# Optimization experiments

Measured on AMD Instinct MI355X. Metric: run time of the kernel, lower is better.

## Reference

```python
import jax, jax.numpy as jnp
import numpy as np

B, S, E, H, Dh = 2, 2048, 1024, 16, 64


def setup_inputs() -> dict:
    key = jax.random.key(0)
    ks = jax.random.split(key, 8)
    w = 0.02
    return {
        "x": jax.random.normal(ks[0], (B, S, E), jnp.float32),
        # torch Linear convention: weight (out, in) = (Dh, E), stacked over heads
        "Wq": jax.random.normal(ks[1], (H, Dh, E), jnp.float32) * w,
        "bq": jax.random.normal(ks[2], (H, Dh), jnp.float32) * w,
        "Wk": jax.random.normal(ks[3], (H, Dh, E), jnp.float32) * w,
        "bk": jax.random.normal(ks[4], (H, Dh), jnp.float32) * w,
        "Wv": jax.random.normal(ks[5], (H, Dh, E), jnp.float32) * w,
        "bv": jax.random.normal(ks[6], (H, Dh), jnp.float32) * w,
        "proj": jax.random.normal(ks[7], (H * Dh, E), jnp.float32) * w,
    }


def reference(x, Wq, bq, Wk, bk, Wv, bv, proj):
    b, s, e = x.shape
    h, dh, _ = Wq.shape
    scale = jnp.sqrt(jnp.asarray(dh, x.dtype))
    # per-head linear projections: y = x @ W.T + b  -> (b, h, s, dh)
    q = jnp.einsum('bse,hde->bhsd', x, Wq) + bq[None, :, None, :]
    k = jnp.einsum('bse,hde->bhsd', x, Wk) + bk[None, :, None, :]
    v = jnp.einsum('bse,hde->bhsd', x, Wv) + bv[None, :, None, :]
    causal = jnp.triu(jnp.ones((s, s), bool), 1)
    scores = jnp.einsum('bhsd,bhtd->bhst', q, k) / scale
    scores = jnp.where(causal[None, None], -jnp.inf, scores)
    # quirk: softmax output divided by sqrt(head_size) a second time
    att = jax.nn.softmax(scores, axis=-1) / scale
    z = jnp.einsum('bhst,bhtd->bhsd', att, v)
    # quirk: torch reshapes (B,H,S,Dh) row-major into (B,S,H*Dh) WITHOUT transpose
    z = z.reshape(b, s, h * dh)
    return z @ proj
```

## Files before the change

kernel.cpp:

```cpp
#include <hip/hip_runtime.h>
#include <hip/hip_bf16.h>

typedef unsigned short u16;
typedef unsigned int u32;
typedef __bf16 bf16x8 __attribute__((ext_vector_type(8)));
typedef float f32x4 __attribute__((ext_vector_type(4)));
typedef u16 u16x8 __attribute__((ext_vector_type(8)));
typedef u16 u16x4 __attribute__((ext_vector_type(4)));
typedef u32 u32x4 __attribute__((ext_vector_type(4)));

#define B_ 2
#define S_ 2048
#define E_ 1024
#define H_ 16
#define Dh_ 64

static __device__ __forceinline__ u16 f2bf(float f) {
  unsigned u = __builtin_bit_cast(unsigned, f);
  u += 0x7fff + ((u >> 16) & 1);
  return (u16)(u >> 16);
}

static __device__ __forceinline__ void gload16(const u16* g, u16* l) {
  __builtin_amdgcn_global_load_lds((const __attribute__((address_space(1))) unsigned int*)g,
                                   (__attribute__((address_space(3))) unsigned int*)l,
                                   16, 0, 0);
}

__global__ void cvt_all(const float* __restrict__ x, const float* __restrict__ wq,
                        const float* __restrict__ wk, const float* __restrict__ wv,
                        u16* __restrict__ xb, u16* __restrict__ wcat) {
  const int i = blockIdx.x * 256 + threadIdx.x;
  const float* src; u16x8* dst;
  if (i < 524288) {
    src = x + (size_t)i * 8;            dst = (u16x8*)xb + i;
  } else {
    const int j = i - 524288;
    dst = (u16x8*)wcat + j;
    if (j < 131072)      src = wq + (size_t)j * 8;
    else if (j < 262144) src = wk + (size_t)(j - 131072) * 8;
    else                 src = wv + (size_t)(j - 262144) * 8;
  }
  float4 a = ((const float4*)src)[0], b = ((const float4*)src)[1];
  u16x8 o;
  o[0] = f2bf(a.x); o[1] = f2bf(a.y); o[2] = f2bf(a.z); o[3] = f2bf(a.w);
  o[4] = f2bf(b.x); o[5] = f2bf(b.y); o[6] = f2bf(b.z); o[7] = f2bf(b.w);
  *dst = o;
}

__global__ void transpose_cvt(const float* __restrict__ in, u16* __restrict__ outT) {
  __shared__ float t[32][33];
  const int e = blockIdx.x * 32 + threadIdx.x;
  const int f = blockIdx.y * 32 + threadIdx.y;
  t[threadIdx.y][threadIdx.x] = in[f * 1024 + e];
  __syncthreads();
  const int eo = blockIdx.x * 32 + threadIdx.y;
  const int fo = blockIdx.y * 32 + threadIdx.x;
  outT[eo * 1024 + fo] = f2bf(t[threadIdx.x][threadIdx.y]);
}

__global__ __launch_bounds__(256) void qkv_gemm(const u16* __restrict__ Wcat,
                                                const u16* __restrict__ Xm,
                                                const float* __restrict__ bq,
                                                const float* __restrict__ bk,
                                                const float* __restrict__ bv,
                                                u16* __restrict__ Qb, u16* __restrict__ Kb,
                                                u16* __restrict__ Vtb, float qs) {
  __shared__ __align__(16) u16 As[2][4096];
  __shared__ __align__(16) u16 Bs[2][4096];
  const int tid = threadIdx.x;
  const int wv = tid >> 6, ln = tid & 63;
  const int lq = ln & 15, lg = ln >> 4;
  const int bid = blockIdx.x;
  const int xcd = bid & 7, within = bid >> 3;
  const int bx = (xcd & 1) * 12 + within % 12;
  const int by = (xcd >> 1) * 8 + within / 12;
  const int ra0 = bx * 128, rb0 = by * 128;
  const int wra = wv >> 1, wrb = wv & 1;

  f32x4 acc[4][4];
  const f32x4 z4 = {0.f, 0.f, 0.f, 0.f};
#pragma unroll
  for (int i = 0; i < 4; ++i)
#pragma unroll
    for (int j = 0; j < 4; ++j) acc[i][j] = z4;

  const int arow = tid >> 2;
  const int acol = (tid & 3) * 8;
  const u16* Ags = Wcat + (ra0 + arow) * 1024 + acol;
  const u16* Bgs = Xm + (rb0 + arow) * 1024 + acol;

#define GSTAGE(KT, BUF) do { const int k0_ = (KT) * 32;              \
    gload16(Ags + k0_,         &As[BUF][wv * 512]);                  \
    gload16(Ags + 65536 + k0_, &As[BUF][wv * 512 + 2048]);           \
    gload16(Bgs + k0_,         &Bs[BUF][wv * 512]);                  \
    gload16(Bgs + 65536 + k0_, &Bs[BUF][wv * 512 + 2048]); } while (0)

  GSTAGE(0, 0);
  for (int kt = 0; kt < 32; ++kt) {
    const int cb = kt & 1;
    if (kt < 31) {
      GSTAGE(kt + 1, cb ^ 1);
      asm volatile("s_waitcnt vmcnt(4)" ::: "memory");
    } else {
      asm volatile("s_waitcnt vmcnt(0)" ::: "memory");
    }
    __builtin_amdgcn_s_barrier();
    __builtin_amdgcn_sched_barrier(0);
    bf16x8 af[4], bfr[4];
#pragma unroll
    for (int i = 0; i < 4; ++i)
      af[i] = *(const bf16x8*)&As[cb][(wra * 64 + i * 16 + lq) * 32 + lg * 8];
#pragma unroll
    for (int j = 0; j < 4; ++j)
      bfr[j] = *(const bf16x8*)&Bs[cb][(wrb * 64 + j * 16 + lq) * 32 + lg * 8];
#pragma unroll
    for (int i = 0; i < 4; ++i)
#pragma unroll
      for (int j = 0; j < 4; ++j)
        acc[i][j] = __builtin_amdgcn_mfma_f32_16x16x32_bf16(af[i], bfr[j], acc[i][j], 0, 0, 0);
    __builtin_amdgcn_sched_barrier(0);
    __builtin_amdgcn_s_barrier();
  }
#undef GSTAGE

  const int region = bx >> 3;
  const float* bias = (region == 0) ? bq : (region == 1) ? bk : bv;
  const float osc = (region == 0) ? qs : 1.0f;
  const int Ar = ra0 + wra * 64, Br = rb0 + wrb * 64;
#pragma unroll
  for (int i = 0; i < 4; ++i) {
#pragma unroll
    for (int j = 0; j < 4; ++j) {
      const int n0 = Ar + i * 16 + lg * 4;
      const int nl = n0 & 1023;
      const int h = nl >> 6, d = nl & 63;
      const int m = Br + j * 16 + lq;
      const int bb = m >> 11, s = m & 2047;
      const float4 b4 = *(const float4*)&bias[nl];
      if (region < 2) {
        u16* out = (region == 0) ? Qb : Kb;
        u16x4 pk;
        pk[0] = f2bf((acc[i][j][0] + b4.x) * osc);
        pk[1] = f2bf((acc[i][j][1] + b4.y) * osc);
        pk[2] = f2bf((acc[i][j][2] + b4.z) * osc);
        pk[3] = f2bf((acc[i][j][3] + b4.w) * osc);
        *(u16x4*)&out[((bb * H_ + h) * S_ + s) * Dh_ + d] = pk;
      } else {
        const float bvv[4] = {b4.x, b4.y, b4.z, b4.w};
#pragma unroll
        for (int r = 0; r < 4; ++r)
          Vtb[((bb * H_ + h) * Dh_ + d + r) * S_ + s] = f2bf(acc[i][j][r] + bvv[r]);
      }
    }
  }
}

__global__ __launch_bounds__(256) void proj_gemm(const u16* __restrict__ Am,
                                                 const u16* __restrict__ Bm,
                                                 float* __restrict__ out) {
  __shared__ __align__(16) u16 As[2][4096];
  __shared__ __align__(16) u16 Bs[2][2048];
  const int tid = threadIdx.x;
  const int wv = tid >> 6, ln = tid & 63;
  const int lq = ln & 15, lg = ln >> 4;
  const int bid = blockIdx.x;
  const int xcd = bid & 7, within = bid >> 3;
  const int bx = within & 7;
  const int by = xcd * 8 + (within >> 3);
  const int ra0 = bx * 128, rb0 = by * 64;
  const int wra = wv >> 1, wrb = wv & 1;

  f32x4 acc[4][2];
  const f32x4 z4 = {0.f, 0.f, 0.f, 0.f};
#pragma unroll
  for (int i = 0; i < 4; ++i)
#pragma unroll
    for (int j = 0; j < 2; ++j) acc[i][j] = z4;

  const int arow = tid >> 2;
  const int acol = (tid & 3) * 8;
  const int brow = wv * 16 + (ln >> 2);
  const int bcol = (ln & 3) * 8;
  const u16* Ags = Am + (ra0 + arow) * 1024 + acol;
  const u16* Bgs = Bm + (rb0 + brow) * 1024 + bcol;

#define PSTAGE(KT, BUF) do { const int k0_ = (KT) * 32;              \
    gload16(Ags + k0_,         &As[BUF][wv * 512]);                  \
    gload16(Ags + 65536 + k0_, &As[BUF][wv * 512 + 2048]);           \
    gload16(Bgs + k0_,         &Bs[BUF][wv * 512]); } while (0)

  PSTAGE(0, 0);
  for (int kt = 0; kt < 32; ++kt) {
    const int cb = kt & 1;
    if (kt < 31) {
      PSTAGE(kt + 1, cb ^ 1);
      asm volatile("s_waitcnt vmcnt(3)" ::: "memory");
    } else {
      asm volatile("s_waitcnt vmcnt(0)" ::: "memory");
    }
    __builtin_amdgcn_s_barrier();
    __builtin_amdgcn_sched_barrier(0);
    bf16x8 af[4], bfr[2];
#pragma unroll
    for (int i = 0; i < 4; ++i)
      af[i] = *(const bf16x8*)&As[cb][(wra * 64 + i * 16 + lq) * 32 + lg * 8];
#pragma unroll
    for (int j = 0; j < 2; ++j)
      bfr[j] = *(const bf16x8*)&Bs[cb][(wrb * 32 + j * 16 + lq) * 32 + lg * 8];
#pragma unroll
    for (int i = 0; i < 4; ++i)
#pragma unroll
      for (int j = 0; j < 2; ++j)
        acc[i][j] = __builtin_amdgcn_mfma_f32_16x16x32_bf16(af[i], bfr[j], acc[i][j], 0, 0, 0);
    __builtin_amdgcn_sched_barrier(0);
    __builtin_amdgcn_s_barrier();
  }
#undef PSTAGE

  const int Ar = ra0 + wra * 64, Br = rb0 + wrb * 32;
#pragma unroll
  for (int i = 0; i < 4; ++i)
#pragma unroll
    for (int j = 0; j < 2; ++j) {
      const int e0 = Ar + i * 16 + lg * 4;
      const int m = Br + j * 16 + lq;
      *(f32x4*)&out[m * 1024 + e0] = acc[i][j];
    }
}

__global__ __launch_bounds__(512, 4) void attn_kernel(const u16* __restrict__ Q,
                                                      const u16* __restrict__ K,
                                                      const u16* __restrict__ Vt,
                                                      u16* __restrict__ Z) {
  __shared__ __align__(16) u16 Ktile[2][8192];
  __shared__ __align__(16) u16 Vtile[2][8192];
  const int tid = threadIdx.x;
  const int wv = tid >> 6, ln = tid & 63;
  const int lq = ln & 15, lg = ln >> 4;
  const bool lgodd = (lg & 1) != 0;
  const int id = blockIdx.x;
  const int within = id >> 3;
  const int xg = id & 7;
  int bh, qt;
  if (within < 32) { bh = xg * 4 + (within >> 4);     qt = 15 - (within & 15); }
  else { const int w = within - 32; bh = xg * 4 + 2 + (w >> 4); qt = w & 15; }
  const int qrow = (qt << 7) + wv * 16 + lq;
  const u16* Qp = Q + (size_t)bh * S_ * Dh_;
  const u16* Kp = K + (size_t)bh * S_ * Dh_;
  const u16* Vp = Vt + (size_t)bh * Dh_ * S_;

  int kgofs[2], vgrow[2], vgcol[2];
#pragma unroll
  for (int j = 0; j < 2; ++j) {
    const int p = j * 512 + tid;
    const int gk = p ^ ((p >> 3) & 7);
    kgofs[j] = (gk >> 3) * 64 + (gk & 7) * 8;
    vgrow[j] = p >> 4;
    vgcol[j] = ((p & 15) ^ ((p >> 4) & 15)) * 8;
  }
  const int sc0 = (lg ^ (lq & 7)) * 8;
  const int sc1 = ((4 + lg) ^ (lq & 7)) * 8;

  bf16x8 qf0 = *(const bf16x8*)&Qp[qrow * Dh_ + lg * 8];
  bf16x8 qf1 = *(const bf16x8*)&Qp[qrow * Dh_ + 32 + lg * 8];

  f32x4 o[4];
  const f32x4 z4 = {0.f, 0.f, 0.f, 0.f};
#pragma unroll
  for (int dt = 0; dt < 4; ++dt) o[dt] = z4;
  float l_lane = 0.f;

#define STAGE(KT, BUF) do { const int kb_ = (KT) * 128;                              \
    gload16(Kp + (size_t)kb_ * 64 + kgofs[0], &Ktile[BUF][wv * 512]);                \
    gload16(Kp + (size_t)kb_ * 64 + kgofs[1], &Ktile[BUF][4096 + wv * 512]);         \
    gload16(Vp + (size_t)vgrow[0] * 2048 + kb_ + vgcol[0], &Vtile[BUF][wv * 512]);   \
    gload16(Vp + (size_t)vgrow[1] * 2048 + kb_ + vgcol[1], &Vtile[BUF][4096 + wv * 512]); \
  } while (0)

  STAGE(0, 0);

  int cur = 0;
  for (int kt = 0; kt <= qt; ++kt) {
    if (kt < qt) {
      STAGE(kt + 1, cur ^ 1);
      asm volatile("s_waitcnt vmcnt(4)" ::: "memory");
    } else {
      asm volatile("s_waitcnt vmcnt(0)" ::: "memory");
    }
    __builtin_amdgcn_s_barrier();
    __builtin_amdgcn_sched_barrier(0);
    const int k0 = kt * 128;
    const bool diag = (kt == qt);
    const int nkk = diag ? ((wv >> 1) + 1) : 4;
#pragma unroll
    for (int kk = 0; kk < 4; ++kk) {
      if (kk < nkk) {
        const int rA = (kk * 32 + lq) * 64;
        const int rB = rA + 1024;
        bf16x8 kA0 = *(const bf16x8*)&Ktile[cur][rA + sc0];
        bf16x8 kA1 = *(const bf16x8*)&Ktile[cur][rA + sc1];
        bf16x8 kB0 = *(const bf16x8*)&Ktile[cur][rB + sc0];
        bf16x8 kB1 = *(const bf16x8*)&Ktile[cur][rB + sc1];
        f32x4 sa = z4, sb = z4;
        __builtin_amdgcn_s_setprio(1);
        sa = __builtin_amdgcn_mfma_f32_16x16x32_bf16(kA0, qf0, sa, 0, 0, 0);
        sa = __builtin_amdgcn_mfma_f32_16x16x32_bf16(kA1, qf1, sa, 0, 0, 0);
        sb = __builtin_amdgcn_mfma_f32_16x16x32_bf16(kB0, qf0, sb, 0, 0, 0);
        sb = __builtin_amdgcn_mfma_f32_16x16x32_bf16(kB1, qf1, sb, 0, 0, 0);
        __builtin_amdgcn_s_setprio(0);
        if (diag) {
          const int keyA = k0 + kk * 32 + lg * 4;
          const int keyB = keyA + 16;
#pragma unroll
          for (int r = 0; r < 4; ++r) {
            if (keyA + r > qrow) sa[r] = -3.0e38f;
            if (keyB + r > qrow) sb[r] = -3.0e38f;
          }
        }
        float e0 = __builtin_amdgcn_exp2f(sa[0]);
        float e1 = __builtin_amdgcn_exp2f(sa[1]);
        float e2 = __builtin_amdgcn_exp2f(sa[2]);
        float e3 = __builtin_amdgcn_exp2f(sa[3]);
        float f0 = __builtin_amdgcn_exp2f(sb[0]);
        float f1 = __builtin_amdgcn_exp2f(sb[1]);
        float f2 = __builtin_amdgcn_exp2f(sb[2]);
        float f3 = __builtin_amdgcn_exp2f(sb[3]);
        l_lane += ((e0 + e1) + (e2 + e3)) + ((f0 + f1) + (f2 + f3));
        u32 A0, A1, B0, B1;
        asm("v_cvt_pk_bf16_f32 %0, %1, %2" : "=v"(A0) : "v"(e0), "v"(e1));
        asm("v_cvt_pk_bf16_f32 %0, %1, %2" : "=v"(A1) : "v"(e2), "v"(e3));
        asm("v_cvt_pk_bf16_f32 %0, %1, %2" : "=v"(B0) : "v"(f0), "v"(f1));
        asm("v_cvt_pk_bf16_f32 %0, %1, %2" : "=v"(B1) : "v"(f2), "v"(f3));
        asm("v_permlane32_swap_b32 %0, %1" : "+v"(A0), "+v"(B0));
        asm("v_permlane32_swap_b32 %0, %1" : "+v"(A1), "+v"(B1));
        const u32 A0x = __shfl_xor((int)A0, 16), B0x = __shfl_xor((int)B0, 16);
        const u32 A1x = __shfl_xor((int)A1, 16), B1x = __shfl_xor((int)B1, 16);
        u32x4 w;
        w[0] = lgodd ? B0x : A0;
        w[1] = lgodd ? B1x : A1;
        w[2] = lgodd ? B0 : A0x;
        w[3] = lgodd ? B1 : A1x;
        const bf16x8 pf = __builtin_bit_cast(bf16x8, w);
        const int scvk = ((kk * 4 + lg) ^ lq) * 8;
        __builtin_amdgcn_s_setprio(1);
#pragma unroll
        for (int dt = 0; dt < 4; ++dt) {
          bf16x8 vf = *(const bf16x8*)&Vtile[cur][(dt * 16 + lq) * 128 + scvk];
          o[dt] = __builtin_amdgcn_mfma_f32_16x16x32_bf16(vf, pf, o[dt], 0, 0, 0);
        }
        __builtin_amdgcn_s_setprio(0);
      }
    }
    __builtin_amdgcn_sched_barrier(0);
    __builtin_amdgcn_s_barrier();
    cur ^= 1;
  }
#undef STAGE

  float l = l_lane;
  l += __shfl_xor(l, 16);
  l += __shfl_xor(l, 32);
  const float inv = 0.125f / l;
#pragma unroll
  for (int dt = 0; dt < 4; ++dt) {
    u16x4 pko;
#pragma unroll
    for (int r = 0; r < 4; ++r) pko[r] = f2bf(o[dt][r] * inv);
    *(u16x4*)&Z[((size_t)bh * S_ + qrow) * Dh_ + dt * 16 + lg * 4] = pko;
  }
}

extern "C" void kernel_launch(void* const* d_in, const int* in_sizes, int n_in,
                              void* d_out, int out_size, void* d_ws, size_t ws_size,
                              hipStream_t stream) {
  const float* x    = (const float*)d_in[0];
  const float* Wq   = (const float*)d_in[1];
  const float* bq   = (const float*)d_in[2];
  const float* Wk   = (const float*)d_in[3];
  const float* bk   = (const float*)d_in[4];
  const float* Wv   = (const float*)d_in[5];
  const float* bv   = (const float*)d_in[6];
  const float* proj = (const float*)d_in[7];
  float* out = (float*)d_out;

  char* p = (char*)d_ws;
  u16* xb   = (u16*)p; p += (size_t)4096 * 1024 * 2;
  u16* wcat = (u16*)p; p += (size_t)3072 * 1024 * 2;
  u16* pjt  = (u16*)p; p += (size_t)1024 * 1024 * 2;
  u16* Qb   = (u16*)p; p += (size_t)4096 * 1024 * 2;
  u16* Kb   = (u16*)p; p += (size_t)4096 * 1024 * 2;
  u16* Vtb  = (u16*)p; p += (size_t)4096 * 1024 * 2;
  u16* Zb   = (u16*)p; p += (size_t)4096 * 1024 * 2;

  cvt_all<<<dim3(3584), dim3(256), 0, stream>>>(x, Wq, Wk, Wv, xb, wcat);
  transpose_cvt<<<dim3(32, 32), dim3(32, 32), 0, stream>>>(proj, pjt);

  const float qs = 0.125f * 1.44269504f;
  qkv_gemm<<<dim3(768), dim3(256), 0, stream>>>(wcat, xb, bq, bk, bv, Qb, Kb, Vtb, qs);

  attn_kernel<<<dim3(512), dim3(512), 0, stream>>>(Qb, Kb, Vtb, Zb);

  proj_gemm<<<dim3(512), dim3(256), 0, stream>>>(pjt, Zb, out);
}
```

Before: 105.0 us.

## Retile QKV GEMM to 256x256 blocks with swizzled LDS and interleaved pipeline

The QKV projection GEMM now uses 256x256 output tiles with 512 threads and a K step of 64, instead of 128x128 tiles with 256 threads. LDS columns are XOR-swizzled to avoid bank conflicts. The loop is split into four phases that interleave LDS reads, prefetching of the next stage and MFMA bursts, with raised priority during the MFMAs. The goal is more arithmetic per byte loaded and better overlap of loads with MFMAs. In exchange the grid shrinks to 192 blocks, fewer than the 256 CUs, and the double-buffered LDS grows to 128KB per block.

```diff
diff --git a/kernel.cpp b/kernel.cpp
--- a/kernel.cpp
+++ b/kernel.cpp
@@ -59,83 +59,130 @@
   outT[eo * 1024 + fo] = f2bf(t[threadIdx.x][threadIdx.y]);
 }
 
-__global__ __launch_bounds__(256) void qkv_gemm(const u16* __restrict__ Wcat,
-                                                const u16* __restrict__ Xm,
-                                                const float* __restrict__ bq,
-                                                const float* __restrict__ bk,
-                                                const float* __restrict__ bv,
-                                                u16* __restrict__ Qb, u16* __restrict__ Kb,
-                                                u16* __restrict__ Vtb, float qs) {
-  __shared__ __align__(16) u16 As[2][4096];
-  __shared__ __align__(16) u16 Bs[2][4096];
+__global__ __launch_bounds__(512, 2) void qkv_gemm(const u16* __restrict__ Wcat,
+                                                   const u16* __restrict__ Xm,
+                                                   const float* __restrict__ bq,
+                                                   const float* __restrict__ bk,
+                                                   const float* __restrict__ bv,
+                                                   u16* __restrict__ Qb, u16* __restrict__ Kb,
+                                                   u16* __restrict__ Vtb, float qs) {
+  __shared__ __align__(16) u16 Alds[2][16384];
+  __shared__ __align__(16) u16 Blds[2][16384];
   const int tid = threadIdx.x;
   const int wv = tid >> 6, ln = tid & 63;
   const int lq = ln & 15, lg = ln >> 4;
+  const int wm = wv >> 2, wn = wv & 3;
   const int bid = blockIdx.x;
-  const int xcd = bid & 7, within = bid >> 3;
-  const int bx = (xcd & 1) * 12 + within % 12;
-  const int by = (xcd >> 1) * 8 + within / 12;
-  const int ra0 = bx * 128, rb0 = by * 128;
-  const int wra = wv >> 1, wrb = wv & 1;
-
-  f32x4 acc[4][4];
+  const int xcd = bid & 7, w = bid >> 3;
+  const int bx = w % 12;
+  const int by = xcd * 2 + w / 12;
+  const int ra0 = bx * 256, rb0 = by * 256;
+
+  const int r_t = tid >> 3, c_t = tid & 7;
+  const int gcol = (c_t ^ (r_t & 7)) * 8;
+  const u16* Asrc = Wcat + (ra0 + r_t) * 1024 + gcol;
+  const u16* Bsrc = Xm   + (rb0 + r_t) * 1024 + gcol;
+
+  const int sc0 = (lg ^ (lq & 7)) * 8;
+  const int sc1 = ((4 + lg) ^ (lq & 7)) * 8;
+  const int baseA = (wm * 128 + lq) * 64;
+  const int baseB = (wn * 64 + lq) * 64;
+
+  f32x4 acc[8][4];
   const f32x4 z4 = {0.f, 0.f, 0.f, 0.f};
 #pragma unroll
-  for (int i = 0; i < 4; ++i)
+  for (int i = 0; i < 8; ++i)
 #pragma unroll
     for (int j = 0; j < 4; ++j) acc[i][j] = z4;
 
-  const int arow = tid >> 2;
-  const int acol = (tid & 3) * 8;
-  const u16* Ags = Wcat + (ra0 + arow) * 1024 + acol;
-  const u16* Bgs = Xm + (rb0 + arow) * 1024 + acol;
-
-#define GSTAGE(KT, BUF) do { const int k0_ = (KT) * 32;              \
-    gload16(Ags + k0_,         &As[BUF][wv * 512]);                  \
-    gload16(Ags + 65536 + k0_, &As[BUF][wv * 512 + 2048]);           \
-    gload16(Bgs + k0_,         &Bs[BUF][wv * 512]);                  \
-    gload16(Bgs + 65536 + k0_, &Bs[BUF][wv * 512 + 2048]); } while (0)
-
-  GSTAGE(0, 0);
-  for (int kt = 0; kt < 32; ++kt) {
-    const int cb = kt & 1;
-    if (kt < 31) {
-      GSTAGE(kt + 1, cb ^ 1);
-      asm volatile("s_waitcnt vmcnt(4)" ::: "memory");
-    } else {
-      asm volatile("s_waitcnt vmcnt(0)" ::: "memory");
-    }
-    __builtin_amdgcn_s_barrier();
-    __builtin_amdgcn_sched_barrier(0);
-    bf16x8 af[4], bfr[4];
-#pragma unroll
-    for (int i = 0; i < 4; ++i)
-      af[i] = *(const bf16x8*)&As[cb][(wra * 64 + i * 16 + lq) * 32 + lg * 8];
-#pragma unroll
-    for (int j = 0; j < 4; ++j)
-      bfr[j] = *(const bf16x8*)&Bs[cb][(wrb * 64 + j * 16 + lq) * 32 + lg * 8];
-#pragma unroll
-    for (int i = 0; i < 4; ++i)
-#pragma unroll
-      for (int j = 0; j < 4; ++j)
-        acc[i][j] = __builtin_amdgcn_mfma_f32_16x16x32_bf16(af[i], bfr[j], acc[i][j], 0, 0, 0);
-    __builtin_amdgcn_sched_barrier(0);
-    __builtin_amdgcn_s_barrier();
-  }
-#undef GSTAGE
-
-  const int region = bx >> 3;
+#define SA(Q, KT, BUF) gload16(Asrc + (Q) * 65536 + (KT) * 64, &Alds[BUF][((Q) * 512 + tid) * 8])
+#define SB(Q, KT, BUF) gload16(Bsrc + (Q) * 65536 + (KT) * 64, &Blds[BUF][((Q) * 512 + tid) * 8])
+#define LOADA(MH, SC) do {                                                         \
+    _Pragma("unroll") for (int ii = 0; ii < 4; ++ii)                               \
+      af[ii] = *(const bf16x8*)&Alds[cb][baseA + (MH) * 4096 + ii * 1024 + (SC)];  \
+  } while (0)
+#define LOADB(DST, SC) do {                                                        \
+    _Pragma("unroll") for (int j = 0; j < 4; ++j)                                  \
+      DST[j] = *(const bf16x8*)&Blds[cb][baseB + j * 1024 + (SC)];                 \
+  } while (0)
+#define MF(MH, BQ) do {                                                            \
+    _Pragma("unroll") for (int ii = 0; ii < 4; ++ii)                               \
+      _Pragma("unroll") for (int j = 0; j < 4; ++j)                                \
+        acc[(MH) * 4 + ii][j] =                                                    \
+            __builtin_amdgcn_mfma_f32_16x16x32_bf16(af[ii], BQ[j],                 \
+                                                    acc[(MH) * 4 + ii][j], 0, 0, 0); \
+  } while (0)
+
+  SB(0, 0, 0); SB(1, 0, 0); SB(2, 0, 0); SB(3, 0, 0);
+  SA(0, 0, 0); SA(2, 0, 0); SA(1, 0, 0); SA(3, 0, 0);
+
+  for (int kt = 0; kt < 16; ++kt) {
+    const int cb = kt & 1, nb = cb ^ 1;
+    const bool st = (kt < 15);
+    asm volatile("s_waitcnt vmcnt(2)" ::: "memory");
+    __builtin_amdgcn_s_barrier();
+    __builtin_amdgcn_sched_barrier(0);
+    bf16x8 af[4], bq0[4], bq1[4];
+    LOADA(0, sc0);
+    LOADB(bq0, sc0);
+    if (st) { SB(0, kt + 1, nb); SB(1, kt + 1, nb); }
+    __builtin_amdgcn_s_barrier();
+    asm volatile("s_waitcnt lgkmcnt(0)" ::: "memory");
+    __builtin_amdgcn_sched_barrier(0);
+    __builtin_amdgcn_s_setprio(1);
+    MF(0, bq0);
+    __builtin_amdgcn_s_setprio(0);
+    __builtin_amdgcn_s_barrier();
+    LOADA(0, sc1);
+    LOADB(bq1, sc1);
+    if (st) { SB(2, kt + 1, nb); SB(3, kt + 1, nb); }
+    __builtin_amdgcn_s_barrier();
+    asm volatile("s_waitcnt lgkmcnt(0)" ::: "memory");
+    __builtin_amdgcn_sched_barrier(0);
+    __builtin_amdgcn_s_setprio(1);
+    MF(0, bq1);
+    __builtin_amdgcn_s_setprio(0);
+    __builtin_amdgcn_s_barrier();
+    if (st) { asm volatile("s_waitcnt vmcnt(4)" ::: "memory"); }
+    else    { asm volatile("s_waitcnt vmcnt(0)" ::: "memory"); }
+    __builtin_amdgcn_s_barrier();
+    __builtin_amdgcn_sched_barrier(0);
+    LOADA(1, sc0);
+    if (st) { SA(0, kt + 1, nb); SA(2, kt + 1, nb); }
+    __builtin_amdgcn_s_barrier();
+    asm volatile("s_waitcnt lgkmcnt(0)" ::: "memory");
+    __builtin_amdgcn_sched_barrier(0);
+    __builtin_amdgcn_s_setprio(1);
+    MF(1, bq0);
+    __builtin_amdgcn_s_setprio(0);
+    __builtin_amdgcn_s_barrier();
+    LOADA(1, sc1);
+    if (st) { SA(1, kt + 1, nb); SA(3, kt + 1, nb); }
+    __builtin_amdgcn_s_barrier();
+    asm volatile("s_waitcnt lgkmcnt(0)" ::: "memory");
+    __builtin_amdgcn_sched_barrier(0);
+    __builtin_amdgcn_s_setprio(1);
+    MF(1, bq1);
+    __builtin_amdgcn_s_setprio(0);
+    __builtin_amdgcn_s_barrier();
+  }
+#undef SA
+#undef SB
+#undef LOADA
+#undef LOADB
+#undef MF
+
+  const int region = bx >> 2;
   const float* bias = (region == 0) ? bq : (region == 1) ? bk : bv;
   const float osc = (region == 0) ? qs : 1.0f;
-  const int Ar = ra0 + wra * 64, Br = rb0 + wrb * 64;
-#pragma unroll
-  for (int i = 0; i < 4; ++i) {
+#pragma unroll
+  for (int i = 0; i < 8; ++i) {
 #pragma unroll
     for (int j = 0; j < 4; ++j) {
-      const int n0 = Ar + i * 16 + lg * 4;
+      const int n0 = ra0 + wm * 128 + (i >> 2) * 64 + (i & 3) * 16 + lg * 4;
       const int nl = n0 & 1023;
       const int h = nl >> 6, d = nl & 63;
-      const int m = Br + j * 16 + lq;
+      const int m = rb0 + wn * 64 + j * 16 + lq;
       const int bb = m >> 11, s = m & 2047;
       const float4 b4 = *(const float4*)&bias[nl];
       if (region < 2) {
@@ -397,7 +444,7 @@
   transpose_cvt<<<dim3(32, 32), dim3(32, 32), 0, stream>>>(proj, pjt);
 
   const float qs = 0.125f * 1.44269504f;
-  qkv_gemm<<<dim3(768), dim3(256), 0, stream>>>(wcat, xb, bq, bk, bv, Qb, Kb, Vtb, qs);
+  qkv_gemm<<<dim3(192), dim3(512), 0, stream>>>(wcat, xb, bq, bk, bv, Qb, Kb, Vtb, qs);
 
   attn_kernel<<<dim3(512), dim3(512), 0, stream>>>(Qb, Kb, Vtb, Zb);
 
```

Measured after the change: 104.6 us. About the same (-0.4%).
